# Kernel optimization log

Hardware: AMD Instinct MI355X
Metric: run time of the kernel (lower is better)

## Reference

```python
import jax, jax.numpy as jnp
import numpy as np
from jax import lax

H_HID, W_HID = 8, 12
N_PAIR = H_HID * W_HID   # 96
NF = 32                  # mlp_nfilters
C_FEAT = 512 + 2         # phi_im channels + (x,y) coords


def _conv_relu(x, w, b):
    # 3x3 conv, stride 1, SAME padding (SingleConvBlock), then ReLU
    y = lax.conv_general_dilated(x, w, (1, 1), 'SAME',
                                 dimension_numbers=('NCHW', 'OIHW', 'NCHW'))
    return jax.nn.relu(y + b[None, :, None, None])


def _maxpool2(x):
    return lax.reduce_window(x, -jnp.inf, lax.max, (1, 1, 2, 2), (1, 1, 2, 2), 'VALID')


def setup_inputs() -> dict:
    key = jax.random.key(0)
    ks = jax.random.split(key, 16)
    d = {}
    d['x'] = jax.random.normal(ks[0], (4, 3, 64, 96), jnp.float32)
    d['sen_embed'] = jax.random.normal(ks[1], (4, 384), jnp.float32)

    def p(k, shape, fan_in):
        return (jax.random.normal(k, shape, jnp.float32) / np.float32(np.sqrt(fan_in)))

    d['enc1_w'] = p(ks[2], (64, 3, 3, 3), 3 * 9);      d['enc1_b'] = p(ks[3], (64,), 64)
    d['enc2_w'] = p(ks[4], (128, 64, 3, 3), 64 * 9);   d['enc2_b'] = p(ks[5], (128,), 128)
    d['enc3_w'] = p(ks[6], (256, 128, 3, 3), 128 * 9); d['enc3_b'] = p(ks[7], (256,), 256)
    d['enc4_w'] = p(ks[8], (512, 256, 3, 3), 256 * 9); d['enc4_b'] = p(ks[9], (512,), 512)
    d['g1_w'] = p(ks[10], (1412, 256), 1412);          d['g1_b'] = p(ks[11], (256,), 256)
    d['g2_w'] = p(ks[12], (256, 256), 256);            d['g2_b'] = p(ks[13], (256,), 256)
    d['g3_w'] = p(ks[14], (256, N_PAIR * NF), 256);    d['g3_b'] = p(ks[15], (N_PAIR * NF,), N_PAIR * NF)
    return d


def _forward(x, sen_embed, enc1_w, enc1_b, enc2_w, enc2_b, enc3_w, enc3_b,
             enc4_w, enc4_b, g1_w, g1_b, g2_w, g2_b, g3_w, g3_b):
    # ---- conv encoder ----
    e1 = _conv_relu(x, enc1_w, enc1_b)                     # [B,64,64,96]
    e2 = _conv_relu(_maxpool2(e1), enc2_w, enc2_b)         # [B,128,32,48]
    e3 = _conv_relu(_maxpool2(e2), enc3_w, enc3_b)         # [B,256,16,24]
    phi_im = _conv_relu(_maxpool2(e3), enc4_w, enc4_b)     # [B,512,8,12]
    B = phi_im.shape[0]

    # ---- coordinate grid (matches torch.meshgrid default 'ij' then reshape) ----
    xc = jnp.linspace(-1.0, 1.0, W_HID, dtype=phi_im.dtype)
    yc = jnp.linspace(-1.0, 1.0, H_HID, dtype=phi_im.dtype)
    xg, yg = jnp.meshgrid(xc, yc, indexing='ij')           # each [12,8]
    coord = jnp.stack([xg.reshape(H_HID, W_HID), yg.reshape(H_HID, W_HID)], axis=0)
    coord = jnp.broadcast_to(coord[None], (B, 2, H_HID, W_HID))

    # per-location features F: [B, n_pair, 514]
    F = jnp.concatenate([phi_im, coord], axis=1).reshape(B, C_FEAT, N_PAIR).transpose(0, 2, 1)

    # ---- all-pairs relation network ----
    # pair feature at (a,c) = concat(F[c], F[a], sen_embed); exploit linearity of first
    # Linear to avoid materializing the [B,n,n,1412] concat tensor (same math).
    A, Bm, Cm = g1_w[:C_FEAT], g1_w[C_FEAT:2 * C_FEAT], g1_w[2 * C_FEAT:]
    u = F @ A                                # i-part,  [B,n,256]
    v = F @ Bm                               # j-part,  [B,n,256]
    ws = sen_embed @ Cm + g1_b               # sentence part, [B,256]
    h1 = jax.nn.relu(u[:, None, :, :] + v[:, :, None, :] + ws[:, None, None, :])  # [B,n,n,256]
    h2 = jax.nn.relu(h1 @ g2_w + g2_b)                                           # [B,n,n,256]
    out = jax.nn.relu(h2 @ g3_w + g3_b)                                          # [B,n,n,3072]

    # sum over all n_pair^2 pairs, reshape to feature map [B,32,8,12]
    phi = out.sum(axis=(1, 2)).reshape(B, NF, H_HID, W_HID)
    return phi


def reference(x, sen_embed, enc1_w, enc1_b, enc2_w, enc2_b, enc3_w, enc3_b,
              enc4_w, enc4_b, g1_w, g1_b, g2_w, g2_b, g3_w, g3_b):
    return _forward(x, sen_embed, enc1_w, enc1_b, enc2_w, enc2_b, enc3_w, enc3_b,
                    enc4_w, enc4_b, g1_w, g1_b, g2_w, g2_b, g3_w, g3_b)
```

## Files before the change

### kernel.cpp

```cpp
#include <hip/hip_runtime.h>
#include <hip/hip_bf16.h>

using bf16 = __hip_bfloat16;
typedef __attribute__((ext_vector_type(8))) short short8;
typedef __attribute__((ext_vector_type(4))) float f32x4;

static __device__ __forceinline__ bf16 f2b(float x) { return __float2bfloat16(x); }
static __device__ __forceinline__ float b2f(bf16 x) { return __bfloat162float(x); }
static __device__ __forceinline__ short fb(float x) {
  bf16 h = __float2bfloat16(fmaxf(x, 0.f));
  return *(short*)&h;
}

static __device__ __forceinline__ void gload_lds16(const void* g, void* l) {
  auto gp = (const __attribute__((address_space(1))) unsigned int*)g;
  auto lp = (__attribute__((address_space(3))) unsigned int*)l;
  __builtin_amdgcn_global_load_lds(gp, lp, 16, 0, 0);
}

__global__ void conv1pool_kernel(const float* __restrict__ x, const float* __restrict__ w,
                                 const float* __restrict__ bias, bf16* __restrict__ out) {
  const int H = 64, W = 96, HW = H * W;
  __shared__ float wl[27 * 64];
  int tid = threadIdx.x;
  for (int idx = tid; idx < 27 * 64; idx += 256) {
    int k = idx >> 6, oc_ = idx & 63;
    wl[idx] = w[oc_ * 27 + k];
  }
  __syncthreads();
  int oc = tid & 63;
  int pp = blockIdx.x * 4 + (tid >> 6);
  int b = pp / 1536, rem = pp - b * 1536;
  int yp = rem / 48, xp = rem - yp * 48;
  int y0 = 2 * yp - 1, x0 = 2 * xp - 1;
  float win[3][4][4];
  #pragma unroll
  for (int ic = 0; ic < 3; ++ic) {
    const float* xsrc = x + ((size_t)b * 3 + ic) * HW;
    #pragma unroll
    for (int dy = 0; dy < 4; ++dy) {
      int yy = y0 + dy;
      #pragma unroll
      for (int dx = 0; dx < 4; ++dx) {
        int xx = x0 + dx;
        win[ic][dy][dx] = (yy >= 0 && yy < H && xx >= 0 && xx < W) ? xsrc[yy * W + xx] : 0.f;
      }
    }
  }
  float cmax = -1e30f;
  #pragma unroll
  for (int sy = 0; sy < 2; ++sy)
    #pragma unroll
    for (int sx = 0; sx < 2; ++sx) {
      float acc = 0.f;
      #pragma unroll
      for (int ic = 0; ic < 3; ++ic)
        #pragma unroll
        for (int ky = 0; ky < 3; ++ky)
          #pragma unroll
          for (int kx = 0; kx < 3; ++kx)
            acc += win[ic][sy + ky][sx + kx] * wl[(ic * 9 + ky * 3 + kx) * 64 + oc];
      cmax = fmaxf(cmax, acc);
    }
  out[(size_t)pp * 64 + oc] = f2b(fmaxf(cmax + bias[oc], 0.f));
}

__global__ void prep_kernel(const float* __restrict__ w2, const float* __restrict__ w3,
                            const float* __restrict__ w4, const float* __restrict__ g1w,
                            const float* __restrict__ sen, float* __restrict__ outz,
                            bf16* __restrict__ w2r, bf16* __restrict__ w3r,
                            bf16* __restrict__ w4r, bf16* __restrict__ wuv,
                            bf16* __restrict__ Fe, float* __restrict__ zb) {
  const int S1 = 73728, S2 = S1 + 294912, S3 = S2 + 1179648, S4 = S3 + 442368,
            S5 = S4 + 12288, S6 = S5 + 24576, S7 = S6 + 36864, S8 = S7 + 64;
  int i = blockIdx.x * 256 + threadIdx.x;
  if (i < S1) {
    int j = i, K = 576, IC = 64;
    int oc = j / K, r = j - oc * K, tap = r / IC, ic = r - tap * IC;
    w2r[j] = f2b(w2[((size_t)oc * IC + ic) * 9 + tap]);
  } else if (i < S2) {
    int j = i - S1, K = 1152, IC = 128;
    int oc = j / K, r = j - oc * K, tap = r / IC, ic = r - tap * IC;
    w3r[j] = f2b(w3[((size_t)oc * IC + ic) * 9 + tap]);
  } else if (i < S3) {
    int j = i - S2, K = 2304, IC = 256;
    int oc = j / K, r = j - oc * K, tap = r / IC, ic = r - tap * IC;
    w4r[j] = f2b(w4[((size_t)oc * IC + ic) * 9 + tap]);
  } else if (i < S4) {
    int j = i - S3;
    int n = j / 576, c = j - n * 576;
    float val = 0.f;
    if (n < 256)      { if (c < 514) val = g1w[(size_t)c * 256 + n]; }
    else if (n < 512) { if (c < 514) val = g1w[(size_t)(514 + c) * 256 + (n - 256)]; }
    else              { if (c < 384) val = g1w[(size_t)(1028 + c) * 256 + (n - 512)]; }
    wuv[j] = f2b(val);
  } else if (i < S5) {
    outz[i - S4] = 0.f;
  } else if (i < S6) {
    int j = i - S5;
    int r = j >> 6, cc = j & 63;
    int p = r % 96;
    float val = 0.f;
    if (cc == 0) val = -1.0f + 2.0f * (float)(p / 8) / 11.0f;
    else if (cc == 1) val = -1.0f + 2.0f * (float)(p % 8) / 7.0f;
    Fe[(size_t)r * 576 + 512 + cc] = f2b(val);
  } else if (i < S7) {
    int j = i - S6;
    int r = j / 576, c = j - r * 576;
    float val = (r < 4 && c < 384) ? sen[r * 384 + c] : 0.f;
    Fe[(size_t)(384 + r) * 576 + c] = f2b(val);
  } else if (i < S8) {
    zb[i - S7] = 0.f;
  }
}

__global__ void transpose2_kernel(const float* __restrict__ g2w, const float* __restrict__ g3w,
                                  bf16* __restrict__ w2t, bf16* __restrict__ w3t) {
  __shared__ bf16 t[32][33];
  int bid = blockIdx.x;
  const float* in;
  bf16* out;
  int R, C, c0, r0;
  if (bid < 64) { in = g2w; out = w2t; R = 256; C = 256; c0 = (bid & 7) * 32; r0 = (bid >> 3) * 32; }
  else { int b2 = bid - 64; in = g3w; out = w3t; R = 256; C = 3072; c0 = (b2 % 96) * 32; r0 = (b2 / 96) * 32; }
  int x = threadIdx.x & 31, y = threadIdx.x >> 5;
  for (int yy = y; yy < 32; yy += 8) {
    int r = r0 + yy, c = c0 + x;
    if (r < R && c < C) t[yy][x] = f2b(in[(size_t)r * C + c]);
  }
  __syncthreads();
  for (int yy = y; yy < 32; yy += 8) {
    int c = c0 + yy, r = r0 + x;
    if (r < R && c < C) out[(size_t)c * R + r] = t[x][yy];
  }
}

template <int CBITS, bool POOL>
__launch_bounds__(256)
__global__ void gemm_conv_kernel(const bf16* __restrict__ pin, const bf16* __restrict__ Wt,
                                 const float* __restrict__ bias, bf16* __restrict__ outb,
                                 const bf16* __restrict__ zbuf,
                                 int Hi, int Wi, int N, int ldout) {
  const int C = 1 << CBITS;
  const int K = 9 << CBITS;
  int m0 = blockIdx.y * 64, n0 = blockIdx.x * 64;
  __shared__ __align__(16) short A_lds[64 * 64];
  __shared__ __align__(16) short B_lds[64 * 64];
  int tid = threadIdx.x, w = tid >> 6, l = tid & 63;
  int quad = l >> 4, l16 = l & 15;
  f32x4 acc[4];
  #pragma unroll
  for (int nt = 0; nt < 4; ++nt)
    #pragma unroll
    for (int e = 0; e < 4; ++e) acc[nt][e] = 0.f;

  int lrow = l >> 3;
  int c_sw = (l & 7) ^ lrow;
  int ybase[2], xbase[2], bidx[2];
  #pragma unroll
  for (int i = 0; i < 2; ++i) {
    int row = m0 + w * 16 + i * 8 + lrow;
    if (POOL) {
      int pg = row >> 2, sub = row & 3;
      int Wh = Wi >> 1, HW2 = (Hi >> 1) * Wh;
      int b = pg / HW2, rem = pg - b * HW2;
      int py = rem / Wh, px = rem - py * Wh;
      bidx[i] = b; ybase[i] = 2 * py + (sub >> 1); xbase[i] = 2 * px + (sub & 1);
    } else {
      int HW = Hi * Wi;
      int b = row / HW, pix = row - b * HW;
      int yy = pix / Wi;
      bidx[i] = b; ybase[i] = yy; xbase[i] = pix - yy * Wi;
    }
  }
  const bf16* bg = Wt + (size_t)(n0 + w * 16 + lrow) * K + c_sw * 8;
  short* al = A_lds + ((size_t)w * 128 + l) * 8;
  short* bl = B_lds + ((size_t)w * 128 + l) * 8;

  for (int kc = 0; kc < K; kc += 64) {
    if (kc) __syncthreads();
    int colt = kc + c_sw * 8;
    int tap = colt >> CBITS, cc = colt & (C - 1);
    int ty = tap / 3, tx = tap - 3 * ty;
    #pragma unroll
    for (int i = 0; i < 2; ++i) {
      int yy = ybase[i] + ty - 1, xx = xbase[i] + tx - 1;
      const bf16* asrc = (yy >= 0 && yy < Hi && xx >= 0 && xx < Wi)
          ? pin + ((((size_t)(bidx[i] * Hi + yy)) * Wi + xx) << CBITS) + cc
          : zbuf;
      gload_lds16(asrc, al + i * 512);
      gload_lds16(bg + kc + (size_t)i * 8 * K, bl + i * 512);
    }
    __syncthreads();
    #pragma unroll
    for (int ks = 0; ks < 64; ks += 32) {
      int cb = (ks >> 3) + quad;
      int mr = w * 16 + l16;
      short8 af = *(const short8*)&A_lds[mr * 64 + ((cb ^ (mr & 7)) * 8)];
      #pragma unroll
      for (int nt = 0; nt < 4; ++nt) {
        int nr = nt * 16 + l16;
        short8 bf = *(const short8*)&B_lds[nr * 64 + ((cb ^ (nr & 7)) * 8)];
        acc[nt] = __builtin_amdgcn_mfma_f32_16x16x32_bf16(af, bf, acc[nt], 0, 0, 0);
      }
    }
  }
  if (POOL) {
    int pg = (m0 + w * 16 + quad * 4) >> 2;
    #pragma unroll
    for (int nt = 0; nt < 4; ++nt) {
      int gcol = n0 + nt * 16 + l16;
      float bv = bias[gcol];
      float m = fmaxf(fmaxf(acc[nt][0], acc[nt][1]), fmaxf(acc[nt][2], acc[nt][3]));
      outb[(size_t)pg * N + gcol] = f2b(fmaxf(m + bv, 0.f));
    }
  } else {
    #pragma unroll
    for (int nt = 0; nt < 4; ++nt) {
      int gcol = n0 + nt * 16 + l16;
      float bv = bias[gcol];
      #pragma unroll
      for (int r = 0; r < 4; ++r) {
        int grow = m0 + w * 16 + quad * 4 + r;
        outb[(size_t)grow * ldout + gcol] = f2b(fmaxf(acc[nt][r] + bv, 0.f));
      }
    }
  }
}

__launch_bounds__(256)
__global__ void gemm64_kernel(const bf16* __restrict__ A, const bf16* __restrict__ Wt,
                              float* __restrict__ outf, int K, int ldout) {
  int m0 = blockIdx.y * 64, n0 = blockIdx.x * 64;
  __shared__ __align__(16) short A_lds[64 * 64];
  __shared__ __align__(16) short B_lds[64 * 64];
  int tid = threadIdx.x, w = tid >> 6, l = tid & 63;
  int quad = l >> 4, l16 = l & 15;
  f32x4 acc[4];
  #pragma unroll
  for (int nt = 0; nt < 4; ++nt)
    #pragma unroll
    for (int e = 0; e < 4; ++e) acc[nt][e] = 0.f;

  int lrow = l >> 3;
  int c_sw = (l & 7) ^ lrow;
  const bf16* ag = A + (size_t)(m0 + w * 16 + lrow) * K + c_sw * 8;
  const bf16* bg = Wt + (size_t)(n0 + w * 16 + lrow) * K + c_sw * 8;
  short* al = A_lds + ((size_t)w * 128 + l) * 8;
  short* bl = B_lds + ((size_t)w * 128 + l) * 8;

  for (int kc = 0; kc < K; kc += 64) {
    if (kc) __syncthreads();
    #pragma unroll
    for (int i = 0; i < 2; ++i) {
      gload_lds16(ag + kc + (size_t)i * 8 * K, al + i * 512);
      gload_lds16(bg + kc + (size_t)i * 8 * K, bl + i * 512);
    }
    __syncthreads();
    #pragma unroll
    for (int ks = 0; ks < 64; ks += 32) {
      int cb = (ks >> 3) + quad;
      int mr = w * 16 + l16;
      short8 af = *(const short8*)&A_lds[mr * 64 + ((cb ^ (mr & 7)) * 8)];
      #pragma unroll
      for (int nt = 0; nt < 4; ++nt) {
        int nr = nt * 16 + l16;
        short8 bf = *(const short8*)&B_lds[nr * 64 + ((cb ^ (nr & 7)) * 8)];
        acc[nt] = __builtin_amdgcn_mfma_f32_16x16x32_bf16(af, bf, acc[nt], 0, 0, 0);
      }
    }
  }
  #pragma unroll
  for (int nt = 0; nt < 4; ++nt) {
    int gcol = n0 + nt * 16 + l16;
    #pragma unroll
    for (int r = 0; r < 4; ++r) {
      int grow = m0 + w * 16 + quad * 4 + r;
      outf[(size_t)grow * ldout + gcol] = acc[nt][r];
    }
  }
}

__launch_bounds__(256)
__global__ void gemm2_kernel(const float* __restrict__ uvws, const float* __restrict__ g1b,
                             const bf16* __restrict__ w2t, const float* __restrict__ g2b,
                             bf16* __restrict__ h2) {
  int b = blockIdx.z;
  int m0 = blockIdx.y * 128;
  int n0 = blockIdx.x * 128;
  __shared__ __align__(16) short A_lds[128 * 64];
  __shared__ __align__(16) short B_lds[128 * 64];
  __shared__ __align__(16) float wsl[256];
  int tid = threadIdx.x, w = tid >> 6, l = tid & 63;
  int quad = l >> 4, l16 = l & 15;
  int mw = (w >> 1) * 64, nw = (w & 1) * 64;
  f32x4 acc[4][4];
  #pragma unroll
  for (int i = 0; i < 4; ++i)
    #pragma unroll
    for (int j = 0; j < 4; ++j)
      #pragma unroll
      for (int e = 0; e < 4; ++e) acc[i][j][e] = 0.f;

  wsl[tid] = uvws[(size_t)(384 + b) * 768 + 512 + tid] + g1b[tid];

  int lrow = l >> 3;
  int c_sw = (l & 7) ^ lrow;
  const bf16* bg = w2t + (size_t)(n0 + w * 32 + lrow) * 256 + c_sw * 8;
  short* bl = B_lds + ((size_t)w * 256 + l) * 8;

  int row = tid >> 1, ks0 = (tid & 1) * 32;
  int m = m0 + row;
  int i_idx = m / 96, j_idx = m - i_idx * 96;
  const float* up = uvws + (size_t)(b * 96 + j_idx) * 768 + ks0;
  const float* vp = uvws + (size_t)(b * 96 + i_idx) * 768 + 256 + ks0;
  __syncthreads();

  for (int kc = 0; kc < 256; kc += 64) {
    if (kc) __syncthreads();
    #pragma unroll
    for (int i = 0; i < 4; ++i)
      gload_lds16(bg + kc + (size_t)i * 8 * 256, bl + i * 512);
    {
      const float4* u4 = (const float4*)(up + kc);
      const float4* v4 = (const float4*)(vp + kc);
      const float4* w4 = (const float4*)&wsl[kc + ks0];
      #pragma unroll
      for (int ch = 0; ch < 4; ++ch) {
        short8 pack;
        #pragma unroll
        for (int q = 0; q < 2; ++q) {
          float4 uu = u4[ch * 2 + q], vv = v4[ch * 2 + q], ww = w4[ch * 2 + q];
          pack[q * 4 + 0] = fb(uu.x + vv.x + ww.x);
          pack[q * 4 + 1] = fb(uu.y + vv.y + ww.y);
          pack[q * 4 + 2] = fb(uu.z + vv.z + ww.z);
          pack[q * 4 + 3] = fb(uu.w + vv.w + ww.w);
        }
        int lc = (ks0 >> 3) + ch;
        *(short8*)&A_lds[row * 64 + ((lc ^ (row & 7)) * 8)] = pack;
      }
    }
    __syncthreads();
    #pragma unroll
    for (int ks = 0; ks < 64; ks += 32) {
      int cb = (ks >> 3) + quad;
      short8 af[4], bfr[4];
      #pragma unroll
      for (int mt = 0; mt < 4; ++mt) {
        int mr = mw + mt * 16 + l16;
        af[mt] = *(const short8*)&A_lds[mr * 64 + ((cb ^ (mr & 7)) * 8)];
      }
      #pragma unroll
      for (int nt = 0; nt < 4; ++nt) {
        int nr = nw + nt * 16 + l16;
        bfr[nt] = *(const short8*)&B_lds[nr * 64 + ((cb ^ (nr & 7)) * 8)];
      }
      #pragma unroll
      for (int mt = 0; mt < 4; ++mt)
        #pragma unroll
        for (int nt = 0; nt < 4; ++nt)
          acc[mt][nt] = __builtin_amdgcn_mfma_f32_16x16x32_bf16(af[mt], bfr[nt], acc[mt][nt], 0, 0, 0);
    }
  }
  bf16* h2b = h2 + (size_t)b * 9216 * 256;
  #pragma unroll
  for (int nt = 0; nt < 4; ++nt) {
    int gcol = n0 + nw + nt * 16 + l16;
    float bias = g2b[gcol];
    #pragma unroll
    for (int mt = 0; mt < 4; ++mt) {
      #pragma unroll
      for (int r = 0; r < 4; ++r) {
        int grow = m0 + mw + mt * 16 + quad * 4 + r;
        h2b[(size_t)grow * 256 + gcol] = f2b(fmaxf(acc[mt][nt][r] + bias, 0.f));
      }
    }
  }
}

__launch_bounds__(256)
__global__ void gemm3_kernel(const bf16* __restrict__ h2, const bf16* __restrict__ w3t,
                             const float* __restrict__ g3b, float* __restrict__ phi) {
  int g = blockIdx.x;
  int x = g & 7, s = g >> 3;
  int grp = s / 24;
  int nIdx = s - grp * 24;
  int mb = grp * 8 + x;
  int b = mb / 72;
  int m0 = (mb - b * 72) * 128;
  int n0 = nIdx * 128;
  __shared__ __align__(16) short A_lds[128 * 64];
  __shared__ __align__(16) short B_lds[128 * 64];
  int tid = threadIdx.x, w = tid >> 6, l = tid & 63;
  int quad = l >> 4, l16 = l & 15;
  int mw = (w >> 1) * 64, nw = (w & 1) * 64;
  f32x4 acc[4][4];
  #pragma unroll
  for (int i = 0; i < 4; ++i)
    #pragma unroll
    for (int j = 0; j < 4; ++j)
      #pragma unroll
      for (int e = 0; e < 4; ++e) acc[i][j][e] = 0.f;

  const int K = 256;
  int lrow = l >> 3;
  int c_sw = (l & 7) ^ lrow;
  const bf16* ag = h2 + (size_t)(b * 9216 + m0 + w * 32 + lrow) * K + c_sw * 8;
  const bf16* bg = w3t + (size_t)(n0 + w * 32 + lrow) * K + c_sw * 8;
  short* al = A_lds + ((size_t)w * 256 + l) * 8;
  short* bl = B_lds + ((size_t)w * 256 + l) * 8;

  for (int kc = 0; kc < K; kc += 64) {
    if (kc) __syncthreads();
    #pragma unroll
    for (int i = 0; i < 4; ++i) {
      gload_lds16(ag + kc + (size_t)i * 8 * K, al + i * 512);
      gload_lds16(bg + kc + (size_t)i * 8 * K, bl + i * 512);
    }
    __syncthreads();
    #pragma unroll
    for (int ks = 0; ks < 64; ks += 32) {
      int cb = (ks >> 3) + quad;
      short8 af[4], bfr[4];
      #pragma unroll
      for (int mt = 0; mt < 4; ++mt) {
        int mr = mw + mt * 16 + l16;
        af[mt] = *(const short8*)&A_lds[mr * 64 + ((cb ^ (mr & 7)) * 8)];
      }
      #pragma unroll
      for (int nt = 0; nt < 4; ++nt) {
        int nr = nw + nt * 16 + l16;
        bfr[nt] = *(const short8*)&B_lds[nr * 64 + ((cb ^ (nr & 7)) * 8)];
      }
      #pragma unroll
      for (int mt = 0; mt < 4; ++mt)
        #pragma unroll
        for (int nt = 0; nt < 4; ++nt)
          acc[mt][nt] = __builtin_amdgcn_mfma_f32_16x16x32_bf16(af[mt], bfr[nt], acc[mt][nt], 0, 0, 0);
    }
  }
  #pragma unroll
  for (int nt = 0; nt < 4; ++nt) {
    int gcol = n0 + nw + nt * 16 + l16;
    float bias = g3b[gcol];
    float s2 = 0.f;
    #pragma unroll
    for (int mt = 0; mt < 4; ++mt)
      #pragma unroll
      for (int r = 0; r < 4; ++r)
        s2 += fmaxf(acc[mt][nt][r] + bias, 0.f);
    s2 += __shfl_xor(s2, 16, 64);
    s2 += __shfl_xor(s2, 32, 64);
    if (quad == 0) atomicAdd(&phi[b * 3072 + gcol], s2);
  }
}

extern "C" void kernel_launch(void* const* d_in, const int* in_sizes, int n_in,
                              void* d_out, int out_size, void* d_ws, size_t ws_size,
                              hipStream_t stream) {
  const float* x   = (const float*)d_in[0];
  const float* sen = (const float*)d_in[1];
  const float* w1  = (const float*)d_in[2];
  const float* b1  = (const float*)d_in[3];
  const float* w2  = (const float*)d_in[4];
  const float* b2  = (const float*)d_in[5];
  const float* w3  = (const float*)d_in[6];
  const float* b3  = (const float*)d_in[7];
  const float* w4  = (const float*)d_in[8];
  const float* b4  = (const float*)d_in[9];
  const float* g1w = (const float*)d_in[10];
  const float* g1b = (const float*)d_in[11];
  const float* g2w = (const float*)d_in[12];
  const float* g2b = (const float*)d_in[13];
  const float* g3w = (const float*)d_in[14];
  const float* g3b = (const float*)d_in[15];
  float* out = (float*)d_out;

  char* wsp = (char*)d_ws;
  size_t off = 0;
  auto alloc = [&](size_t bytes) {
    char* p = wsp + off;
    off += (bytes + 255) & ~(size_t)255;
    return (void*)p;
  };
  bf16* p1   = (bf16*)alloc((size_t)6144 * 64 * 2);
  bf16* p2   = (bf16*)alloc((size_t)1536 * 128 * 2);
  bf16* p3   = (bf16*)alloc((size_t)384 * 256 * 2);
  bf16* Fe   = (bf16*)alloc((size_t)448 * 576 * 2);
  bf16* wuv  = (bf16*)alloc((size_t)768 * 576 * 2);
  float* uvws = (float*)alloc((size_t)448 * 768 * 4);
  bf16* w2r  = (bf16*)alloc((size_t)128 * 576 * 2);
  bf16* w3r  = (bf16*)alloc((size_t)256 * 1152 * 2);
  bf16* w4r  = (bf16*)alloc((size_t)512 * 2304 * 2);
  bf16* w2t  = (bf16*)alloc((size_t)256 * 256 * 2);
  bf16* w3t  = (bf16*)alloc((size_t)3072 * 256 * 2);
  bf16* h2   = (bf16*)alloc((size_t)4 * 9216 * 256 * 2);
  float* zbuf = (float*)alloc((size_t)256);

  prep_kernel<<<dim3(8065), 256, 0, stream>>>(w2, w3, w4, g1w, sen, out, w2r, w3r, w4r, wuv, Fe, zbuf);
  transpose2_kernel<<<dim3(832), 256, 0, stream>>>(g2w, g3w, w2t, w3t);

  conv1pool_kernel<<<dim3(1536), 256, 0, stream>>>(x, w1, b1, p1);
  gemm_conv_kernel<6, true><<<dim3(2, 96), 256, 0, stream>>>(p1, w2r, b2, p2, (const bf16*)zbuf, 32, 48, 128, 128);
  gemm_conv_kernel<7, true><<<dim3(4, 24), 256, 0, stream>>>(p2, w3r, b3, p3, (const bf16*)zbuf, 16, 24, 256, 256);
  gemm_conv_kernel<8, false><<<dim3(8, 6), 256, 0, stream>>>(p3, w4r, b4, Fe, (const bf16*)zbuf, 8, 12, 512, 576);

  gemm64_kernel<<<dim3(12, 7), 256, 0, stream>>>(Fe, wuv, uvws, 576, 768);
  gemm2_kernel<<<dim3(2, 72, 4), 256, 0, stream>>>(uvws, g1b, w2t, g2b, h2);
  gemm3_kernel<<<dim3(6912), 256, 0, stream>>>(h2, w3t, g3b, out);
}
```

Measured before the change: 248.1 us.

## Merge prep, transpose and conv1 kernels; double-buffer LDS in conv and gemm64 GEMMs

Folds the weight-prep, transpose and first conv+pool kernels into one launch using block-index ranges, removing two kernel launches and their serialization gaps. The im2col conv GEMMs and gemm64 now double-buffer their A/B LDS tiles, issuing the next K-chunk's global-to-LDS loads before computing the current chunk, with one barrier per iteration instead of two. This doubles LDS use per block. The merged kernel also makes every block allocate both shared arrays and has divergent per-block roles.

```diff
diff --git a/kernel.cpp b/kernel.cpp
--- a/kernel.cpp
+++ b/kernel.cpp
@@ -18,120 +18,121 @@
   __builtin_amdgcn_global_load_lds(gp, lp, 16, 0, 0);
 }
 
-__global__ void conv1pool_kernel(const float* __restrict__ x, const float* __restrict__ w,
-                                 const float* __restrict__ bias, bf16* __restrict__ out) {
-  const int H = 64, W = 96, HW = H * W;
+__global__ void prep_all_kernel(const float* __restrict__ x, const float* __restrict__ w1,
+                                const float* __restrict__ b1, bf16* __restrict__ p1,
+                                const float* __restrict__ w2, const float* __restrict__ w3,
+                                const float* __restrict__ w4, const float* __restrict__ g1w,
+                                const float* __restrict__ sen, float* __restrict__ outz,
+                                bf16* __restrict__ w2r, bf16* __restrict__ w3r,
+                                bf16* __restrict__ w4r, bf16* __restrict__ wuv,
+                                bf16* __restrict__ Fe, float* __restrict__ zb,
+                                const float* __restrict__ g2w, const float* __restrict__ g3w,
+                                bf16* __restrict__ w2t, bf16* __restrict__ w3t) {
   __shared__ float wl[27 * 64];
+  __shared__ bf16 tt[32][33];
+  int bid = blockIdx.x;
   int tid = threadIdx.x;
-  for (int idx = tid; idx < 27 * 64; idx += 256) {
-    int k = idx >> 6, oc_ = idx & 63;
-    wl[idx] = w[oc_ * 27 + k];
-  }
-  __syncthreads();
-  int oc = tid & 63;
-  int pp = blockIdx.x * 4 + (tid >> 6);
-  int b = pp / 1536, rem = pp - b * 1536;
-  int yp = rem / 48, xp = rem - yp * 48;
-  int y0 = 2 * yp - 1, x0 = 2 * xp - 1;
-  float win[3][4][4];
-  #pragma unroll
-  for (int ic = 0; ic < 3; ++ic) {
-    const float* xsrc = x + ((size_t)b * 3 + ic) * HW;
-    #pragma unroll
-    for (int dy = 0; dy < 4; ++dy) {
-      int yy = y0 + dy;
-      #pragma unroll
-      for (int dx = 0; dx < 4; ++dx) {
-        int xx = x0 + dx;
-        win[ic][dy][dx] = (yy >= 0 && yy < H && xx >= 0 && xx < W) ? xsrc[yy * W + xx] : 0.f;
-      }
-    }
-  }
-  float cmax = -1e30f;
-  #pragma unroll
-  for (int sy = 0; sy < 2; ++sy)
-    #pragma unroll
-    for (int sx = 0; sx < 2; ++sx) {
-      float acc = 0.f;
-      #pragma unroll
-      for (int ic = 0; ic < 3; ++ic)
+  if (bid < 1536) {
+    const int H = 64, W = 96, HW = H * W;
+    for (int idx = tid; idx < 27 * 64; idx += 256) {
+      int k = idx >> 6, oc_ = idx & 63;
+      wl[idx] = w1[oc_ * 27 + k];
+    }
+    __syncthreads();
+    int oc = tid & 63;
+    int pp = bid * 4 + (tid >> 6);
+    int b = pp / 1536, rem = pp - b * 1536;
+    int yp = rem / 48, xp = rem - yp * 48;
+    int y0 = 2 * yp - 1, x0 = 2 * xp - 1;
+    float win[3][4][4];
+    #pragma unroll
+    for (int ic = 0; ic < 3; ++ic) {
+      const float* xsrc = x + ((size_t)b * 3 + ic) * HW;
+      #pragma unroll
+      for (int dy = 0; dy < 4; ++dy) {
+        int yy = y0 + dy;
         #pragma unroll
-        for (int ky = 0; ky < 3; ++ky)
+        for (int dx = 0; dx < 4; ++dx) {
+          int xx = x0 + dx;
+          win[ic][dy][dx] = (yy >= 0 && yy < H && xx >= 0 && xx < W) ? xsrc[yy * W + xx] : 0.f;
+        }
+      }
+    }
+    float cmax = -1e30f;
+    #pragma unroll
+    for (int sy = 0; sy < 2; ++sy)
+      #pragma unroll
+      for (int sx = 0; sx < 2; ++sx) {
+        float acc = 0.f;
+        #pragma unroll
+        for (int ic = 0; ic < 3; ++ic)
           #pragma unroll
-          for (int kx = 0; kx < 3; ++kx)
-            acc += win[ic][sy + ky][sx + kx] * wl[(ic * 9 + ky * 3 + kx) * 64 + oc];
-      cmax = fmaxf(cmax, acc);
-    }
-  out[(size_t)pp * 64 + oc] = f2b(fmaxf(cmax + bias[oc], 0.f));
-}
-
-__global__ void prep_kernel(const float* __restrict__ w2, const float* __restrict__ w3,
-                            const float* __restrict__ w4, const float* __restrict__ g1w,
-                            const float* __restrict__ sen, float* __restrict__ outz,
-                            bf16* __restrict__ w2r, bf16* __restrict__ w3r,
-                            bf16* __restrict__ w4r, bf16* __restrict__ wuv,
-                            bf16* __restrict__ Fe, float* __restrict__ zb) {
-  const int S1 = 73728, S2 = S1 + 294912, S3 = S2 + 1179648, S4 = S3 + 442368,
-            S5 = S4 + 12288, S6 = S5 + 24576, S7 = S6 + 36864, S8 = S7 + 64;
-  int i = blockIdx.x * 256 + threadIdx.x;
-  if (i < S1) {
-    int j = i, K = 576, IC = 64;
-    int oc = j / K, r = j - oc * K, tap = r / IC, ic = r - tap * IC;
-    w2r[j] = f2b(w2[((size_t)oc * IC + ic) * 9 + tap]);
-  } else if (i < S2) {
-    int j = i - S1, K = 1152, IC = 128;
-    int oc = j / K, r = j - oc * K, tap = r / IC, ic = r - tap * IC;
-    w3r[j] = f2b(w3[((size_t)oc * IC + ic) * 9 + tap]);
-  } else if (i < S3) {
-    int j = i - S2, K = 2304, IC = 256;
-    int oc = j / K, r = j - oc * K, tap = r / IC, ic = r - tap * IC;
-    w4r[j] = f2b(w4[((size_t)oc * IC + ic) * 9 + tap]);
-  } else if (i < S4) {
-    int j = i - S3;
-    int n = j / 576, c = j - n * 576;
-    float val = 0.f;
-    if (n < 256)      { if (c < 514) val = g1w[(size_t)c * 256 + n]; }
-    else if (n < 512) { if (c < 514) val = g1w[(size_t)(514 + c) * 256 + (n - 256)]; }
-    else              { if (c < 384) val = g1w[(size_t)(1028 + c) * 256 + (n - 512)]; }
-    wuv[j] = f2b(val);
-  } else if (i < S5) {
-    outz[i - S4] = 0.f;
-  } else if (i < S6) {
-    int j = i - S5;
-    int r = j >> 6, cc = j & 63;
-    int p = r % 96;
-    float val = 0.f;
-    if (cc == 0) val = -1.0f + 2.0f * (float)(p / 8) / 11.0f;
-    else if (cc == 1) val = -1.0f + 2.0f * (float)(p % 8) / 7.0f;
-    Fe[(size_t)r * 576 + 512 + cc] = f2b(val);
-  } else if (i < S7) {
-    int j = i - S6;
-    int r = j / 576, c = j - r * 576;
-    float val = (r < 4 && c < 384) ? sen[r * 384 + c] : 0.f;
-    Fe[(size_t)(384 + r) * 576 + c] = f2b(val);
-  } else if (i < S8) {
-    zb[i - S7] = 0.f;
-  }
-}
-
-__global__ void transpose2_kernel(const float* __restrict__ g2w, const float* __restrict__ g3w,
-                                  bf16* __restrict__ w2t, bf16* __restrict__ w3t) {
-  __shared__ bf16 t[32][33];
-  int bid = blockIdx.x;
-  const float* in;
-  bf16* out;
-  int R, C, c0, r0;
-  if (bid < 64) { in = g2w; out = w2t; R = 256; C = 256; c0 = (bid & 7) * 32; r0 = (bid >> 3) * 32; }
-  else { int b2 = bid - 64; in = g3w; out = w3t; R = 256; C = 3072; c0 = (b2 % 96) * 32; r0 = (b2 / 96) * 32; }
-  int x = threadIdx.x & 31, y = threadIdx.x >> 5;
-  for (int yy = y; yy < 32; yy += 8) {
-    int r = r0 + yy, c = c0 + x;
-    if (r < R && c < C) t[yy][x] = f2b(in[(size_t)r * C + c]);
-  }
-  __syncthreads();
-  for (int yy = y; yy < 32; yy += 8) {
-    int c = c0 + yy, r = r0 + x;
-    if (r < R && c < C) out[(size_t)c * R + r] = t[x][yy];
+          for (int ky = 0; ky < 3; ++ky)
+            #pragma unroll
+            for (int kx = 0; kx < 3; ++kx)
+              acc += win[ic][sy + ky][sx + kx] * wl[(ic * 9 + ky * 3 + kx) * 64 + oc];
+        cmax = fmaxf(cmax, acc);
+      }
+    p1[(size_t)pp * 64 + oc] = f2b(fmaxf(cmax + b1[oc], 0.f));
+  } else if (bid < 9601) {
+    const int S1 = 73728, S2 = S1 + 294912, S3 = S2 + 1179648, S4 = S3 + 442368,
+              S5 = S4 + 12288, S6 = S5 + 24576, S7 = S6 + 36864, S8 = S7 + 64;
+    int i = (bid - 1536) * 256 + tid;
+    if (i < S1) {
+      int j = i, K = 576, IC = 64;
+      int oc = j / K, r = j - oc * K, tap = r / IC, ic = r - tap * IC;
+      w2r[j] = f2b(w2[((size_t)oc * IC + ic) * 9 + tap]);
+    } else if (i < S2) {
+      int j = i - S1, K = 1152, IC = 128;
+      int oc = j / K, r = j - oc * K, tap = r / IC, ic = r - tap * IC;
+      w3r[j] = f2b(w3[((size_t)oc * IC + ic) * 9 + tap]);
+    } else if (i < S3) {
+      int j = i - S2, K = 2304, IC = 256;
+      int oc = j / K, r = j - oc * K, tap = r / IC, ic = r - tap * IC;
+      w4r[j] = f2b(w4[((size_t)oc * IC + ic) * 9 + tap]);
+    } else if (i < S4) {
+      int j = i - S3;
+      int n = j / 576, c = j - n * 576;
+      float val = 0.f;
+      if (n < 256)      { if (c < 514) val = g1w[(size_t)c * 256 + n]; }
+      else if (n < 512) { if (c < 514) val = g1w[(size_t)(514 + c) * 256 + (n - 256)]; }
+      else              { if (c < 384) val = g1w[(size_t)(1028 + c) * 256 + (n - 512)]; }
+      wuv[j] = f2b(val);
+    } else if (i < S5) {
+      outz[i - S4] = 0.f;
+    } else if (i < S6) {
+      int j = i - S5;
+      int r = j >> 6, cc = j & 63;
+      int p = r % 96;
+      float val = 0.f;
+      if (cc == 0) val = -1.0f + 2.0f * (float)(p / 8) / 11.0f;
+      else if (cc == 1) val = -1.0f + 2.0f * (float)(p % 8) / 7.0f;
+      Fe[(size_t)r * 576 + 512 + cc] = f2b(val);
+    } else if (i < S7) {
+      int j = i - S6;
+      int r = j / 576, c = j - r * 576;
+      float val = (r < 4 && c < 384) ? sen[r * 384 + c] : 0.f;
+      Fe[(size_t)(384 + r) * 576 + c] = f2b(val);
+    } else if (i < S8) {
+      zb[i - S7] = 0.f;
+    }
+  } else {
+    int b2 = bid - 9601;
+    const float* in;
+    bf16* out;
+    int R = 256, C, c0, r0;
+    if (b2 < 64) { in = g2w; out = w2t; C = 256; c0 = (b2 & 7) * 32; r0 = (b2 >> 3) * 32; }
+    else { b2 -= 64; in = g3w; out = w3t; C = 3072; c0 = (b2 % 96) * 32; r0 = (b2 / 96) * 32; }
+    int xq = tid & 31, yq = tid >> 5;
+    for (int yy = yq; yy < 32; yy += 8) {
+      int r = r0 + yy, c = c0 + xq;
+      if (r < R && c < C) tt[yy][xq] = f2b(in[(size_t)r * C + c]);
+    }
+    __syncthreads();
+    for (int yy = yq; yy < 32; yy += 8) {
+      int c = c0 + yy, r = r0 + xq;
+      if (r < R && c < C) out[(size_t)c * R + r] = tt[xq][yy];
+    }
   }
 }
 
@@ -144,8 +145,8 @@
   const int C = 1 << CBITS;
   const int K = 9 << CBITS;
   int m0 = blockIdx.y * 64, n0 = blockIdx.x * 64;
-  __shared__ __align__(16) short A_lds[64 * 64];
-  __shared__ __align__(16) short B_lds[64 * 64];
+  __shared__ __align__(16) short A_lds[2][64 * 64];
+  __shared__ __align__(16) short B_lds[2][64 * 64];
   int tid = threadIdx.x, w = tid >> 6, l = tid & 63;
   int quad = l >> 4, l16 = l & 15;
   f32x4 acc[4];
@@ -174,14 +175,13 @@
     }
   }
   const bf16* bg = Wt + (size_t)(n0 + w * 16 + lrow) * K + c_sw * 8;
-  short* al = A_lds + ((size_t)w * 128 + l) * 8;
-  short* bl = B_lds + ((size_t)w * 128 + l) * 8;
-
-  for (int kc = 0; kc < K; kc += 64) {
-    if (kc) __syncthreads();
+
+  auto stage = [&](int kc, int buf) {
     int colt = kc + c_sw * 8;
     int tap = colt >> CBITS, cc = colt & (C - 1);
     int ty = tap / 3, tx = tap - 3 * ty;
+    short* al = &A_lds[buf][((size_t)w * 128 + l) * 8];
+    short* bl = &B_lds[buf][((size_t)w * 128 + l) * 8];
     #pragma unroll
     for (int i = 0; i < 2; ++i) {
       int yy = ybase[i] + ty - 1, xx = xbase[i] + tx - 1;
@@ -191,17 +191,24 @@
       gload_lds16(asrc, al + i * 512);
       gload_lds16(bg + kc + (size_t)i * 8 * K, bl + i * 512);
     }
+  };
+
+  stage(0, 0);
+  const int NK = K >> 6;
+  for (int ik = 0; ik < NK; ++ik) {
+    int buf = ik & 1;
     __syncthreads();
+    if (ik + 1 < NK) stage((ik + 1) * 64, buf ^ 1);
     #pragma unroll
     for (int ks = 0; ks < 64; ks += 32) {
       int cb = (ks >> 3) + quad;
       int mr = w * 16 + l16;
-      short8 af = *(const short8*)&A_lds[mr * 64 + ((cb ^ (mr & 7)) * 8)];
+      short8 af = *(const short8*)&A_lds[buf][mr * 64 + ((cb ^ (mr & 7)) * 8)];
       #pragma unroll
       for (int nt = 0; nt < 4; ++nt) {
         int nr = nt * 16 + l16;
-        short8 bf = *(const short8*)&B_lds[nr * 64 + ((cb ^ (nr & 7)) * 8)];
-        acc[nt] = __builtin_amdgcn_mfma_f32_16x16x32_bf16(af, bf, acc[nt], 0, 0, 0);
+        short8 bf2 = *(const short8*)&B_lds[buf][nr * 64 + ((cb ^ (nr & 7)) * 8)];
+        acc[nt] = __builtin_amdgcn_mfma_f32_16x16x32_bf16(af, bf2, acc[nt], 0, 0, 0);
       }
     }
   }
@@ -232,8 +239,8 @@
 __global__ void gemm64_kernel(const bf16* __restrict__ A, const bf16* __restrict__ Wt,
                               float* __restrict__ outf, int K, int ldout) {
   int m0 = blockIdx.y * 64, n0 = blockIdx.x * 64;
-  __shared__ __align__(16) short A_lds[64 * 64];
-  __shared__ __align__(16) short B_lds[64 * 64];
+  __shared__ __align__(16) short A_lds[2][64 * 64];
+  __shared__ __align__(16) short B_lds[2][64 * 64];
   int tid = threadIdx.x, w = tid >> 6, l = tid & 63;
   int quad = l >> 4, l16 = l & 15;
   f32x4 acc[4];
@@ -246,27 +253,33 @@
   int c_sw = (l & 7) ^ lrow;
   const bf16* ag = A + (size_t)(m0 + w * 16 + lrow) * K + c_sw * 8;
   const bf16* bg = Wt + (size_t)(n0 + w * 16 + lrow) * K + c_sw * 8;
-  short* al = A_lds + ((size_t)w * 128 + l) * 8;
-  short* bl = B_lds + ((size_t)w * 128 + l) * 8;
-
-  for (int kc = 0; kc < K; kc += 64) {
-    if (kc) __syncthreads();
+
+  auto stage = [&](int kc, int buf) {
+    short* al = &A_lds[buf][((size_t)w * 128 + l) * 8];
+    short* bl = &B_lds[buf][((size_t)w * 128 + l) * 8];
     #pragma unroll
     for (int i = 0; i < 2; ++i) {
       gload_lds16(ag + kc + (size_t)i * 8 * K, al + i * 512);
       gload_lds16(bg + kc + (size_t)i * 8 * K, bl + i * 512);
     }
+  };
+
+  stage(0, 0);
+  const int NK = K >> 6;
+  for (int ik = 0; ik < NK; ++ik) {
+    int buf = ik & 1;
     __syncthreads();
+    if (ik + 1 < NK) stage((ik + 1) * 64, buf ^ 1);
     #pragma unroll
     for (int ks = 0; ks < 64; ks += 32) {
       int cb = (ks >> 3) + quad;
       int mr = w * 16 + l16;
-      short8 af = *(const short8*)&A_lds[mr * 64 + ((cb ^ (mr & 7)) * 8)];
+      short8 af = *(const short8*)&A_lds[buf][mr * 64 + ((cb ^ (mr & 7)) * 8)];
       #pragma unroll
       for (int nt = 0; nt < 4; ++nt) {
         int nr = nt * 16 + l16;
-        short8 bf = *(const short8*)&B_lds[nr * 64 + ((cb ^ (nr & 7)) * 8)];
-        acc[nt] = __builtin_amdgcn_mfma_f32_16x16x32_bf16(af, bf, acc[nt], 0, 0, 0);
+        short8 bf2 = *(const short8*)&B_lds[buf][nr * 64 + ((cb ^ (nr & 7)) * 8)];
+        acc[nt] = __builtin_amdgcn_mfma_f32_16x16x32_bf16(af, bf2, acc[nt], 0, 0, 0);
       }
     }
   }
@@ -497,10 +510,9 @@
   bf16* h2   = (bf16*)alloc((size_t)4 * 9216 * 256 * 2);
   float* zbuf = (float*)alloc((size_t)256);
 
-  prep_kernel<<<dim3(8065), 256, 0, stream>>>(w2, w3, w4, g1w, sen, out, w2r, w3r, w4r, wuv, Fe, zbuf);
-  transpose2_kernel<<<dim3(832), 256, 0, stream>>>(g2w, g3w, w2t, w3t);
-
-  conv1pool_kernel<<<dim3(1536), 256, 0, stream>>>(x, w1, b1, p1);
+  prep_all_kernel<<<dim3(10433), 256, 0, stream>>>(x, w1, b1, p1, w2, w3, w4, g1w, sen, out,
+                                                   w2r, w3r, w4r, wuv, Fe, zbuf, g2w, g3w, w2t, w3t);
+
   gemm_conv_kernel<6, true><<<dim3(2, 96), 256, 0, stream>>>(p1, w2r, b2, p2, (const bf16*)zbuf, 32, 48, 128, 128);
   gemm_conv_kernel<7, true><<<dim3(4, 24), 256, 0, stream>>>(p2, w3r, b3, p3, (const bf16*)zbuf, 16, 24, 256, 256);
   gemm_conv_kernel<8, false><<<dim3(8, 6), 256, 0, stream>>>(p3, w4r, b4, Fe, (const bf16*)zbuf, 8, 12, 512, 576);
```

New measurement: 240.7 us. -3.0%, faster.
